# Kernel optimization log

Hardware: AMD Instinct MI355X
Metric: run time of the kernel (lower is better)

Reference implementation:

```python
import jax, jax.numpy as jnp
import numpy as np

MUL = 32
HEAD_DIM = 16
CLIP = 5.0
EPS = 1e-6
INV_SQRTD = 1.0 / np.sqrt(HEAD_DIM)
ENV_BLOCKS = (1, 3)          # 0e, 1o
TP_BLOCKS = (1, 1, 3, 3)     # 0e(0x0), 0e(1x1), 1o(0x1), 1o(1x0)


def so3_layernorm(x, g, block_dims):
    """x: [..., MUL, D]; per-irrep-block RMS norm over (mul, components), affine scale g [MUL, n_blocks]."""
    out, i = [], 0
    for b, d in enumerate(block_dims):
        blk = x[..., i:i + d]
        n = jnp.sqrt(jnp.mean(blk * blk, axis=(-2, -1), keepdims=True) + EPS)
        out.append(blk / n * g[:, b][:, None])
        i += d
    return jnp.concatenate(out, axis=-1)


def scatter_softmax(logits, seg, num_segments):
    """softmax over edges grouped by destination node. logits [E, M]."""
    m = jax.ops.segment_max(logits, seg, num_segments=num_segments)
    e = jnp.exp(logits - m[seg])
    d = jax.ops.segment_sum(e, seg, num_segments=num_segments)
    return e / d[seg]


def setup_inputs() -> dict:
    key = jax.random.key(0)
    ks = jax.random.split(key, 16)
    N, E, LAT, NODE_DIM, COND, HID = 16384, 262144, 64, 64, 32, 128
    sc = lambda f: f ** -0.5
    return {
        "node_attrs": jax.random.normal(ks[0], (N, NODE_DIM), jnp.float32),
        "scalar_state": jax.random.normal(ks[1], (E, LAT), jnp.float32),
        "equiv_state": jax.random.normal(ks[2], (E, MUL, 4), jnp.float32),
        "edge_conditioning": jax.random.normal(ks[3], (E, COND), jnp.float32),
        "residual_update_coeff": jax.random.uniform(ks[4], (1,), jnp.float32),
        "W_env1": jax.random.normal(ks[5], (LAT + COND, HID), jnp.float32) * sc(LAT + COND),
        "b_env1": jnp.zeros((HID,), jnp.float32),
        "W_env2": jax.random.normal(ks[6], (HID, MUL * 2), jnp.float32) * sc(HID),
        "Wq": jax.random.normal(ks[7], (NODE_DIM, MUL * HEAD_DIM), jnp.float32) * sc(NODE_DIM),
        "Wk": jax.random.normal(ks[8], (LAT, MUL * HEAD_DIM), jnp.float32) * sc(LAT),
        "g_env": jnp.ones((MUL, 2), jnp.float32),
        "g_tp": jnp.ones((MUL, 4), jnp.float32),
        "Wp1": jax.random.normal(ks[9], (MUL * 2 + COND, HID), jnp.float32) * sc(MUL * 2 + COND),
        "bp1": jnp.zeros((HID,), jnp.float32),
        "Wp2": jax.random.normal(ks[10], (HID, LAT + MUL * 4), jnp.float32) * sc(HID),
        "edge_src": jax.random.randint(ks[11], (E,), 0, N),
    }


def reference(node_attrs, scalar_state, equiv_state, edge_conditioning,
              residual_update_coeff, W_env1, b_env1, W_env2, Wq, Wk,
              g_env, g_tp, Wp1, bp1, Wp2, edge_src):
    N = node_attrs.shape[0]
    E = scalar_state.shape[0]
    LAT = scalar_state.shape[1]

    # --- env_embed_mlp: scalar MLP -> per-(mul, irrep-block) gates on equiv state ---
    x = jnp.concatenate([scalar_state, edge_conditioning], axis=-1)
    h = jax.nn.silu(x @ W_env1 + b_env1)
    w = (h @ W_env2).reshape(E, MUL, 2)                    # [E, mul, 2 blocks]
    w_exp = jnp.repeat(w, np.array(ENV_BLOCKS), axis=-1, total_repeat_length=4)
    env_edges = equiv_state * w_exp                        # [E, mul, 4]

    # --- attention: edge-gathered query, clipped logits, scatter softmax ---
    Q = (node_attrs[edge_src] @ Wq).reshape(E, MUL, HEAD_DIM)
    K = (scalar_state @ Wk).reshape(E, MUL, HEAD_DIM)
    logits = jnp.einsum('emd,emd->em', Q, K) * INV_SQRTD
    logits = jnp.clip(logits, -CLIP, CLIP)
    attn = scatter_softmax(logits, edge_src, N)            # [E, mul]
    env_edges = env_edges * attn[..., None]

    # --- scatter-sum to nodes, SO3 layernorm, gather back ---
    env_nodes = jax.ops.segment_sum(env_edges, edge_src, num_segments=N)  # [N, mul, 4]
    env_nodes = so3_layernorm(env_nodes, g_env, ENV_BLOCKS)
    edge_local_env = env_nodes[edge_src]                   # [E, mul, 4]

    # --- Contracter, uuu mode, instructions: 0x0->0, 1x1->0, 0x1->1, 1x0->1 ---
    s1, v1 = equiv_state[..., 0], equiv_state[..., 1:4]
    s2, v2 = edge_local_env[..., 0], edge_local_env[..., 1:4]
    o0a = s1 * s2                                          # 0e
    o0b = jnp.einsum('emi,emi->em', v1, v2) / np.sqrt(3.0) # 0e (CG of 1x1->0)
    o1a = s1[..., None] * v2                               # 1o
    o1b = v1 * s2[..., None]                               # 1o
    tp_out = jnp.concatenate([o0a[..., None], o0b[..., None], o1a, o1b], axis=-1)  # [E, mul, 8]
    tp_out = so3_layernorm(tp_out, g_tp, TP_BLOCKS)

    # --- projection: scalar MLP -> new scalar latent + per-path weights mixing equiv blocks ---
    scalars = tp_out[..., :2].reshape(E, MUL * 2)
    xp = jnp.concatenate([scalars, edge_conditioning], axis=-1)
    hp = jax.nn.silu(xp @ Wp1 + bp1)
    op = hp @ Wp2
    new_scalar = op[:, :LAT]
    pw = op[:, LAT:].reshape(E, MUL, 4)
    new_s = pw[..., 0] * tp_out[..., 0] + pw[..., 1] * tp_out[..., 1]
    new_v = pw[..., 2:3] * tp_out[..., 2:5] + pw[..., 3:4] * tp_out[..., 5:8]
    new_equiv = jnp.concatenate([new_s[..., None], new_v], axis=-1)  # [E, mul, 4]

    # --- residual streams ---
    c_old = jax.lax.rsqrt(residual_update_coeff ** 2 + 1.0)
    c_new = residual_update_coeff * c_old
    scalar_out = c_old * scalar_state + c_new * new_scalar
    equiv_out = c_old * equiv_state + c_new * new_equiv
    return scalar_out, equiv_out
```

## Files before the change

kernel.cpp:

```cpp
#include <hip/hip_runtime.h>
#include <math.h>

#define EPSF 1e-6f
#define STX 100
#define STH 132

__device__ __forceinline__ float silu_f(float x){ return x * (1.0f/(1.0f + __expf(-x))); }

__global__ __launch_bounds__(256) void k_qnode(
    const float* __restrict__ na, const float* __restrict__ Wq,
    float* __restrict__ qn)
{
  __shared__ float At[64*16];
  const int nb = blockIdx.x * 16;
  const int t = threadIdx.x;
  for (int f = t; f < 16*64; f += 256){ int n = f>>6, i = f&63; At[i*16+n] = na[(size_t)(nb+n)*64 + i]; }
  __syncthreads();
  float acc0[16], acc1[16];
#pragma unroll
  for (int n=0;n<16;n++){ acc0[n]=0.f; acc1[n]=0.f; }
  for (int i=0;i<64;i++){
    float w0 = Wq[(size_t)i*512 + t];
    float w1 = Wq[(size_t)i*512 + t + 256];
#pragma unroll
    for (int n=0;n<16;n++){ float a = At[i*16+n]; acc0[n] = fmaf(a,w0,acc0[n]); acc1[n] = fmaf(a,w1,acc1[n]); }
  }
#pragma unroll
  for (int n=0;n<16;n++){
    qn[(size_t)(nb+n)*512 + t]       = acc0[n];
    qn[(size_t)(nb+n)*512 + t + 256] = acc1[n];
  }
}

__global__ __launch_bounds__(256) void k_hist(
    const int* __restrict__ esrc, int E, int* __restrict__ cnt)
{
  int i = blockIdx.x*256 + threadIdx.x;
  if (i < E) atomicAdd(cnt + esrc[i], 1);
}

__global__ __launch_bounds__(1024) void k_scan(
    int* __restrict__ cnt_cur, int N, int* __restrict__ off)
{
  __shared__ int part[1024];
  const int t = threadIdx.x;
  const int ipt = (N + 1023) >> 10;
  int s = 0;
  for (int k=0;k<ipt;k++){ int i = t*ipt + k; if (i < N) s += cnt_cur[i]; }
  part[t] = s;
  __syncthreads();
  for (int d=1; d<1024; d<<=1){
    int v = (t >= d) ? part[t-d] : 0;
    __syncthreads();
    part[t] += v;
    __syncthreads();
  }
  int run = (t==0) ? 0 : part[t-1];
  for (int k=0;k<ipt;k++){
    int i = t*ipt + k;
    if (i < N){ int c = cnt_cur[i]; off[i] = run; cnt_cur[i] = run; run += c; }
  }
  if (t == 1023) off[N] = part[1023];
}

__global__ __launch_bounds__(256) void k_scatter(
    const int* __restrict__ esrc, int E, int* __restrict__ cur, int* __restrict__ perm)
{
  int i = blockIdx.x*256 + threadIdx.x;
  if (i < E){ int p = atomicAdd(cur + esrc[i], 1); perm[p] = i; }
}

__global__ __launch_bounds__(256,4) void k_edge1(
    const float* __restrict__ ssi, const float* __restrict__ cond,
    const int* __restrict__ esrc,
    const float* __restrict__ W1, const float* __restrict__ b1,
    const float* __restrict__ W2, const float* __restrict__ Wk,
    const float* __restrict__ qn,
    float* __restrict__ elw)
{
  __shared__ float Xs[32*STX];
  __shared__ float Hs[32*STH];
  __shared__ float lg[32*32];
  __shared__ int src_l[32];
  const int e0 = blockIdx.x * 32;
  const int t = threadIdx.x;
  const int r0 = (t>>5)*4;

  if (t < 32) src_l[t] = esrc[e0+t];
  for (int f=t; f<512; f+=256){ int r=f>>4, q=(f&15)*4;
    *(float4*)(Xs + r*STX + q) = *(const float4*)(ssi + (size_t)(e0+r)*64 + q); }
  { int f=t; int r=f>>3, q=(f&7)*4;
    *(float4*)(Xs + r*STX + 64 + q) = *(const float4*)(cond + (size_t)(e0+r)*32 + q); }
  __syncthreads();

  {
    const int c0 = (t&31)*4;
    float acc[4][4] = {};
    for (int i0=0;i0<96;i0+=4){
      float4 wv[4], xv[4];
#pragma unroll
      for (int k=0;k<4;k++) wv[k] = *(const float4*)(W1 + (size_t)(i0+k)*128 + c0);
#pragma unroll
      for (int rr=0;rr<4;rr++) xv[rr] = *(const float4*)(Xs + (r0+rr)*STX + i0);
#pragma unroll
      for (int rr=0;rr<4;rr++){
        const float xs[4] = {xv[rr].x,xv[rr].y,xv[rr].z,xv[rr].w};
#pragma unroll
        for (int k=0;k<4;k++){
          acc[rr][0] = fmaf(xs[k], wv[k].x, acc[rr][0]);
          acc[rr][1] = fmaf(xs[k], wv[k].y, acc[rr][1]);
          acc[rr][2] = fmaf(xs[k], wv[k].z, acc[rr][2]);
          acc[rr][3] = fmaf(xs[k], wv[k].w, acc[rr][3]);
        }
      }
    }
    const float4 bb = *(const float4*)(b1 + c0);
#pragma unroll
    for (int rr=0;rr<4;rr++){
      float4 h;
      h.x = silu_f(acc[rr][0]+bb.x); h.y = silu_f(acc[rr][1]+bb.y);
      h.z = silu_f(acc[rr][2]+bb.z); h.w = silu_f(acc[rr][3]+bb.w);
      *(float4*)(Hs + (r0+rr)*STH + c0) = h;
    }
  }
  __syncthreads();

  float wacc[4][2] = {};
  {
    const int c0 = (t&31)*2;
    for (int j0=0;j0<128;j0+=4){
      float2 w2[4]; float4 hv[4];
#pragma unroll
      for (int k=0;k<4;k++) w2[k] = *(const float2*)(W2 + (size_t)(j0+k)*64 + c0);
#pragma unroll
      for (int rr=0;rr<4;rr++) hv[rr] = *(const float4*)(Hs + (r0+rr)*STH + j0);
#pragma unroll
      for (int rr=0;rr<4;rr++){
        const float hs[4] = {hv[rr].x,hv[rr].y,hv[rr].z,hv[rr].w};
#pragma unroll
        for (int k=0;k<4;k++){
          wacc[rr][0] = fmaf(hs[k], w2[k].x, wacc[rr][0]);
          wacc[rr][1] = fmaf(hs[k], w2[k].y, wacc[rr][1]);
        }
      }
    }
  }
  __syncthreads();
  float* wl = Hs;
  {
    const int c0 = (t&31)*2;
#pragma unroll
    for (int rr=0;rr<4;rr++)
      *(float2*)(wl + (r0+rr)*66 + c0) = make_float2(wacc[rr][0], wacc[rr][1]);
  }

  for (int it=0; it<4; it++){
    const int c0k = (t&31)*4 + it*128;
    float acc[4][4] = {};
    for (int i0=0;i0<64;i0+=4){
      float4 wv[4], xv[4];
#pragma unroll
      for (int k=0;k<4;k++) wv[k] = *(const float4*)(Wk + (size_t)(i0+k)*512 + c0k);
#pragma unroll
      for (int rr=0;rr<4;rr++) xv[rr] = *(const float4*)(Xs + (r0+rr)*STX + i0);
#pragma unroll
      for (int rr=0;rr<4;rr++){
        const float xs[4] = {xv[rr].x,xv[rr].y,xv[rr].z,xv[rr].w};
#pragma unroll
        for (int k=0;k<4;k++){
          acc[rr][0] = fmaf(xs[k], wv[k].x, acc[rr][0]);
          acc[rr][1] = fmaf(xs[k], wv[k].y, acc[rr][1]);
          acc[rr][2] = fmaf(xs[k], wv[k].z, acc[rr][2]);
          acc[rr][3] = fmaf(xs[k], wv[k].w, acc[rr][3]);
        }
      }
    }
    const int m = ((t&31)>>2) + it*8;
#pragma unroll
    for (int rr=0;rr<4;rr++){
      const float4 q = *(const float4*)(qn + (size_t)src_l[r0+rr]*512 + c0k);
      float p = acc[rr][0]*q.x + acc[rr][1]*q.y + acc[rr][2]*q.z + acc[rr][3]*q.w;
      p += __shfl_xor(p, 1);
      p += __shfl_xor(p, 2);
      if ((t&3)==0) lg[(r0+rr)*32 + m] = p;
    }
  }
  __syncthreads();

  for (int f=t; f<1024; f+=256){
    int r=f>>5, m=f&31;
    float l = lg[f] * 0.25f;
    l = fminf(5.0f, fmaxf(-5.0f, l));
    const float el = __expf(l);
    const size_t b = (size_t)(e0+r)*96;
    elw[b + m]      = el;
    elw[b + 32 + m] = el * wl[r*66 + 2*m];
    elw[b + 64 + m] = el * wl[r*66 + 2*m+1];
  }
}

__global__ __launch_bounds__(128) void k_env(
    const float* __restrict__ elw, const float* __restrict__ equiv,
    const int* __restrict__ perm, const int* __restrict__ off,
    const float* __restrict__ g_env, float* __restrict__ envn)
{
  __shared__ float red[128];
  __shared__ float inv0s, inv1s;
  const int n = blockIdx.x, t = threadIdx.x;
  const int m = t>>2, c = t&3;
  const int j0 = off[n], j1 = off[n+1];
  float den = 0.f, acc = 0.f;
  for (int j=j0; j<j1; j++){
    const int pe = perm[j];
    const size_t b = (size_t)pe*96;
    const float el = elw[b + m];
    const float a  = elw[b + (c ? 64 : 32) + m];
    const float ev = equiv[((size_t)pe*32 + m)*4 + c];
    den += el;
    acc = fmaf(a, ev, acc);
  }
  const float x = (den > 0.f) ? acc/den : 0.f;
  red[t] = x*x;
  __syncthreads();
  if (t < 32){
    float p0 = red[4*t];
    float p1 = red[4*t+1]+red[4*t+2]+red[4*t+3];
#pragma unroll
    for (int k=1;k<32;k<<=1){ p0 += __shfl_xor(p0,k); p1 += __shfl_xor(p1,k); }
    if (t==0){ inv0s = 1.0f/sqrtf(p0*(1.0f/32.0f) + EPSF); inv1s = 1.0f/sqrtf(p1*(1.0f/96.0f) + EPSF); }
  }
  __syncthreads();
  const float g = g_env[m*2 + (c?1:0)];
  envn[(size_t)n*128 + t] = x * (c ? inv1s : inv0s) * g;
}

__global__ __launch_bounds__(256,4) void k_edge1_atm(
    const float* __restrict__ ssi, const float* __restrict__ cond,
    const float* __restrict__ equiv, const int* __restrict__ esrc,
    const float* __restrict__ W1, const float* __restrict__ b1,
    const float* __restrict__ W2, const float* __restrict__ Wk,
    const float* __restrict__ qn,
    float* __restrict__ denom, float* __restrict__ num)
{
  __shared__ float Xs[32*STX];
  __shared__ float Hs[32*STH];
  __shared__ float lg[32*32];
  __shared__ int src_l[32];
  const int e0 = blockIdx.x * 32;
  const int t = threadIdx.x;
  const int r0 = (t>>5)*4;

  if (t < 32) src_l[t] = esrc[e0+t];
  for (int f=t; f<512; f+=256){ int r=f>>4, q=(f&15)*4;
    *(float4*)(Xs + r*STX + q) = *(const float4*)(ssi + (size_t)(e0+r)*64 + q); }
  { int f=t; int r=f>>3, q=(f&7)*4;
    *(float4*)(Xs + r*STX + 64 + q) = *(const float4*)(cond + (size_t)(e0+r)*32 + q); }
  __syncthreads();

  {
    const int c0 = (t&31)*4;
    float acc[4][4] = {};
    for (int i0=0;i0<96;i0+=4){
      float4 wv[4], xv[4];
#pragma unroll
      for (int k=0;k<4;k++) wv[k] = *(const float4*)(W1 + (size_t)(i0+k)*128 + c0);
#pragma unroll
      for (int rr=0;rr<4;rr++) xv[rr] = *(const float4*)(Xs + (r0+rr)*STX + i0);
#pragma unroll
      for (int rr=0;rr<4;rr++){
        const float xs[4] = {xv[rr].x,xv[rr].y,xv[rr].z,xv[rr].w};
#pragma unroll
        for (int k=0;k<4;k++){
          acc[rr][0] = fmaf(xs[k], wv[k].x, acc[rr][0]);
          acc[rr][1] = fmaf(xs[k], wv[k].y, acc[rr][1]);
          acc[rr][2] = fmaf(xs[k], wv[k].z, acc[rr][2]);
          acc[rr][3] = fmaf(xs[k], wv[k].w, acc[rr][3]);
        }
      }
    }
    const float4 bb = *(const float4*)(b1 + c0);
#pragma unroll
    for (int rr=0;rr<4;rr++){
      float4 h;
      h.x = silu_f(acc[rr][0]+bb.x); h.y = silu_f(acc[rr][1]+bb.y);
      h.z = silu_f(acc[rr][2]+bb.z); h.w = silu_f(acc[rr][3]+bb.w);
      *(float4*)(Hs + (r0+rr)*STH + c0) = h;
    }
  }
  __syncthreads();

  float wacc[4][2] = {};
  {
    const int c0 = (t&31)*2;
    for (int j0=0;j0<128;j0+=4){
      float2 w2[4]; float4 hv[4];
#pragma unroll
      for (int k=0;k<4;k++) w2[k] = *(const float2*)(W2 + (size_t)(j0+k)*64 + c0);
#pragma unroll
      for (int rr=0;rr<4;rr++) hv[rr] = *(const float4*)(Hs + (r0+rr)*STH + j0);
#pragma unroll
      for (int rr=0;rr<4;rr++){
        const float hs[4] = {hv[rr].x,hv[rr].y,hv[rr].z,hv[rr].w};
#pragma unroll
        for (int k=0;k<4;k++){
          wacc[rr][0] = fmaf(hs[k], w2[k].x, wacc[rr][0]);
          wacc[rr][1] = fmaf(hs[k], w2[k].y, wacc[rr][1]);
        }
      }
    }
  }
  __syncthreads();
  float* wl = Hs;
  {
    const int c0 = (t&31)*2;
#pragma unroll
    for (int rr=0;rr<4;rr++)
      *(float2*)(wl + (r0+rr)*66 + c0) = make_float2(wacc[rr][0], wacc[rr][1]);
  }

  for (int it=0; it<4; it++){
    const int c0k = (t&31)*4 + it*128;
    float acc[4][4] = {};
    for (int i0=0;i0<64;i0+=4){
      float4 wv[4], xv[4];
#pragma unroll
      for (int k=0;k<4;k++) wv[k] = *(const float4*)(Wk + (size_t)(i0+k)*512 + c0k);
#pragma unroll
      for (int rr=0;rr<4;rr++) xv[rr] = *(const float4*)(Xs + (r0+rr)*STX + i0);
#pragma unroll
      for (int rr=0;rr<4;rr++){
        const float xs[4] = {xv[rr].x,xv[rr].y,xv[rr].z,xv[rr].w};
#pragma unroll
        for (int k=0;k<4;k++){
          acc[rr][0] = fmaf(xs[k], wv[k].x, acc[rr][0]);
          acc[rr][1] = fmaf(xs[k], wv[k].y, acc[rr][1]);
          acc[rr][2] = fmaf(xs[k], wv[k].z, acc[rr][2]);
          acc[rr][3] = fmaf(xs[k], wv[k].w, acc[rr][3]);
        }
      }
    }
    const int m = ((t&31)>>2) + it*8;
#pragma unroll
    for (int rr=0;rr<4;rr++){
      const float4 q = *(const float4*)(qn + (size_t)src_l[r0+rr]*512 + c0k);
      float p = acc[rr][0]*q.x + acc[rr][1]*q.y + acc[rr][2]*q.z + acc[rr][3]*q.w;
      p += __shfl_xor(p, 1);
      p += __shfl_xor(p, 2);
      if ((t&3)==0) lg[(r0+rr)*32 + m] = p;
    }
  }
  __syncthreads();

  for (int f=t; f<1024; f+=256){
    int r=f>>5, m=f&31;
    float l = lg[f] * 0.25f;
    l = fminf(5.0f, fmaxf(-5.0f, l));
    float el = __expf(l);
    lg[f] = el;
    atomicAdd(denom + (size_t)src_l[r]*32 + m, el);
  }
  __syncthreads();

  for (int f=t; f<1024; f+=256){
    int r=f>>5, m=f&31;
    const float el = lg[r*32+m];
    const float w0 = wl[r*66 + 2*m]   * el;
    const float w1 = wl[r*66 + 2*m+1] * el;
    const float4 ev = *(const float4*)(equiv + ((size_t)(e0+r)*32 + m)*4);
    float* np = num + (size_t)src_l[r]*128 + 4*m;
    atomicAdd(np+0, w0*ev.x);
    atomicAdd(np+1, w1*ev.y);
    atomicAdd(np+2, w1*ev.z);
    atomicAdd(np+3, w1*ev.w);
  }
}

__global__ __launch_bounds__(128) void k_dnorm(
    float* __restrict__ num, const float* __restrict__ denom,
    const float* __restrict__ g_env)
{
  __shared__ float red[128];
  __shared__ float inv0s, inv1s;
  const int n = blockIdx.x, t = threadIdx.x;
  const int m = t>>2, c = t&3;
  const float d = denom[(size_t)n*32+m];
  const float x = (d > 0.0f) ? num[(size_t)n*128+t]/d : 0.0f;
  red[t] = x*x;
  __syncthreads();
  if (t < 32){
    float p0 = red[4*t];
    float p1 = red[4*t+1]+red[4*t+2]+red[4*t+3];
#pragma unroll
    for (int k=1;k<32;k<<=1){ p0 += __shfl_xor(p0,k); p1 += __shfl_xor(p1,k); }
    if (t==0){ inv0s = 1.0f/sqrtf(p0*(1.0f/32.0f) + EPSF); inv1s = 1.0f/sqrtf(p1*(1.0f/96.0f) + EPSF); }
  }
  __syncthreads();
  const float g = g_env[m*2 + (c?1:0)];
  num[(size_t)n*128+t] = x * (c ? inv1s : inv0s) * g;
}

__global__ __launch_bounds__(256,3) void k_edge2(
    const float* __restrict__ ssi, const float* __restrict__ cond,
    const float* __restrict__ equiv, const int* __restrict__ esrc,
    const float* __restrict__ envn, const float* __restrict__ g_tp,
    const float* __restrict__ Wp1, const float* __restrict__ bp1,
    const float* __restrict__ Wp2, const float* __restrict__ ruc,
    float* __restrict__ outs, float* __restrict__ oute)
{
  __shared__ float envl[32*STH];
  __shared__ float Xp[32*STX];
  __shared__ float Hp[32*STH];
  __shared__ float inv_l[32*4];
  __shared__ int src_l[32];
  const int e0 = blockIdx.x * 32;
  const int t = threadIdx.x;
  const int r0 = (t>>5)*4;
  if (t < 32) src_l[t] = esrc[e0+t];
  __syncthreads();
  for (int f=t; f<1024; f+=256){ int r=f>>5, q=(f&31)*4;
    *(float4*)(envl + r*STH + q) = *(const float4*)(envn + (size_t)src_l[r]*128 + q); }
  { int f=t; int r=f>>3, q=(f&7)*4;
    *(float4*)(Xp + r*STX + 64 + q) = *(const float4*)(cond + (size_t)(e0+r)*32 + q); }
  __syncthreads();

  {
    const int r = t>>3, sub = t&7;
    float ss0=0,ss1=0,ss2=0,ss3=0;
#pragma unroll
    for (int mm=0;mm<4;mm++){
      const int m = sub*4+mm;
      const float4 e4 = *(const float4*)(equiv + ((size_t)(e0+r)*32 + m)*4);
      const float4 n4 = *(const float4*)(envl + r*STH + 4*m);
      const float tp0 = e4.x*n4.x;
      const float dv  = e4.y*n4.y + e4.z*n4.z + e4.w*n4.w;
      const float tp1 = dv*0.5773502691896258f;
      ss0 += tp0*tp0;
      ss1 += tp1*tp1;
      ss2 += e4.x*e4.x*(n4.y*n4.y + n4.z*n4.z + n4.w*n4.w);
      ss3 += n4.x*n4.x*(e4.y*e4.y + e4.z*e4.z + e4.w*e4.w);
    }
#pragma unroll
    for (int k=1;k<8;k<<=1){
      ss0 += __shfl_xor(ss0,k); ss1 += __shfl_xor(ss1,k);
      ss2 += __shfl_xor(ss2,k); ss3 += __shfl_xor(ss3,k);
    }
    if (sub == 0){
      inv_l[r*4+0] = 1.0f/sqrtf(ss0*(1.0f/32.0f) + EPSF);
      inv_l[r*4+1] = 1.0f/sqrtf(ss1*(1.0f/32.0f) + EPSF);
      inv_l[r*4+2] = 1.0f/sqrtf(ss2*(1.0f/96.0f) + EPSF);
      inv_l[r*4+3] = 1.0f/sqrtf(ss3*(1.0f/96.0f) + EPSF);
    }
  }
  __syncthreads();

  for (int f=t; f<2048; f+=256){
    const int r = f>>6, col = f&63, m = col>>1;
    const float4 e4 = *(const float4*)(equiv + ((size_t)(e0+r)*32 + m)*4);
    const float4 n4 = *(const float4*)(envl + r*STH + 4*m);
    float v;
    if (col & 1)
      v = (e4.y*n4.y + e4.z*n4.z + e4.w*n4.w)*0.5773502691896258f * inv_l[r*4+1] * g_tp[m*4+1];
    else
      v = e4.x*n4.x * inv_l[r*4+0] * g_tp[m*4+0];
    Xp[r*STX + col] = v;
  }
  __syncthreads();

  {
    const int c0 = (t&31)*4;
    float acc[4][4] = {};
    for (int i0=0;i0<96;i0+=4){
      float4 wv[4], xv[4];
#pragma unroll
      for (int k=0;k<4;k++) wv[k] = *(const float4*)(Wp1 + (size_t)(i0+k)*128 + c0);
#pragma unroll
      for (int rr=0;rr<4;rr++) xv[rr] = *(const float4*)(Xp + (r0+rr)*STX + i0);
#pragma unroll
      for (int rr=0;rr<4;rr++){
        const float xs[4] = {xv[rr].x,xv[rr].y,xv[rr].z,xv[rr].w};
#pragma unroll
        for (int k=0;k<4;k++){
          acc[rr][0] = fmaf(xs[k], wv[k].x, acc[rr][0]);
          acc[rr][1] = fmaf(xs[k], wv[k].y, acc[rr][1]);
          acc[rr][2] = fmaf(xs[k], wv[k].z, acc[rr][2]);
          acc[rr][3] = fmaf(xs[k], wv[k].w, acc[rr][3]);
        }
      }
    }
    const float4 bb = *(const float4*)(bp1 + c0);
#pragma unroll
    for (int rr=0;rr<4;rr++){
      float4 h;
      h.x = silu_f(acc[rr][0]+bb.x); h.y = silu_f(acc[rr][1]+bb.y);
      h.z = silu_f(acc[rr][2]+bb.z); h.w = silu_f(acc[rr][3]+bb.w);
      *(float4*)(Hp + (r0+rr)*STH + c0) = h;
    }
  }
  __syncthreads();

  const float rv = ruc[0];
  const float c_old = 1.0f/sqrtf(rv*rv + 1.0f);
  const float c_new = rv * c_old;

  {
    const int c0 = (t&31)*2;
    float acc[4][2] = {};
    for (int j0=0;j0<128;j0+=4){
      float2 w2[4]; float4 hv[4];
#pragma unroll
      for (int k=0;k<4;k++) w2[k] = *(const float2*)(Wp2 + (size_t)(j0+k)*192 + c0);
#pragma unroll
      for (int rr=0;rr<4;rr++) hv[rr] = *(const float4*)(Hp + (r0+rr)*STH + j0);
#pragma unroll
      for (int rr=0;rr<4;rr++){
        const float hs[4] = {hv[rr].x,hv[rr].y,hv[rr].z,hv[rr].w};
#pragma unroll
        for (int k=0;k<4;k++){
          acc[rr][0] = fmaf(hs[k], w2[k].x, acc[rr][0]);
          acc[rr][1] = fmaf(hs[k], w2[k].y, acc[rr][1]);
        }
      }
    }
#pragma unroll
    for (int rr=0;rr<4;rr++){
      const size_t e = (size_t)(e0+r0+rr);
      const float2 s2 = *(const float2*)(ssi + e*64 + c0);
      float2 o2; o2.x = c_old*s2.x + c_new*acc[rr][0]; o2.y = c_old*s2.y + c_new*acc[rr][1];
      *(float2*)(outs + e*64 + c0) = o2;
    }
  }

  {
    const int m = t&31;
    float acc[4][4] = {};
    for (int j0=0;j0<128;j0+=4){
      float4 w4[4]; float4 hv[4];
#pragma unroll
      for (int k=0;k<4;k++) w4[k] = *(const float4*)(Wp2 + (size_t)(j0+k)*192 + 64 + 4*m);
#pragma unroll
      for (int rr=0;rr<4;rr++) hv[rr] = *(const float4*)(Hp + (r0+rr)*STH + j0);
#pragma unroll
      for (int rr=0;rr<4;rr++){
        const float hs[4] = {hv[rr].x,hv[rr].y,hv[rr].z,hv[rr].w};
#pragma unroll
        for (int k=0;k<4;k++){
          acc[rr][0] = fmaf(hs[k], w4[k].x, acc[rr][0]);
          acc[rr][1] = fmaf(hs[k], w4[k].y, acc[rr][1]);
          acc[rr][2] = fmaf(hs[k], w4[k].z, acc[rr][2]);
          acc[rr][3] = fmaf(hs[k], w4[k].w, acc[rr][3]);
        }
      }
    }
    const float g2 = g_tp[m*4+2], g3 = g_tp[m*4+3];
#pragma unroll
    for (int rr=0;rr<4;rr++){
      const int r = r0+rr;
      const size_t e = (size_t)(e0+r);
      const float4 e4 = *(const float4*)(equiv + (e*32 + m)*4);
      const float4 n4 = *(const float4*)(envl + r*STH + 4*m);
      const float tpn0 = Xp[r*STX + 2*m];
      const float tpn1 = Xp[r*STX + 2*m+1];
      const float a2 = acc[rr][2]*inv_l[r*4+2]*g2;
      const float a3 = acc[rr][3]*inv_l[r*4+3]*g3;
      float4 o;
      o.x = c_old*e4.x + c_new*(acc[rr][0]*tpn0 + acc[rr][1]*tpn1);
      o.y = c_old*e4.y + c_new*(a2*(e4.x*n4.y) + a3*(e4.y*n4.x));
      o.z = c_old*e4.z + c_new*(a2*(e4.x*n4.z) + a3*(e4.z*n4.x));
      o.w = c_old*e4.w + c_new*(a2*(e4.x*n4.w) + a3*(e4.w*n4.x));
      *(float4*)(oute + e*128 + 4*m) = o;
    }
  }
}

extern "C" void kernel_launch(void* const* d_in, const int* in_sizes, int n_in,
                              void* d_out, int out_size, void* d_ws, size_t ws_size,
                              hipStream_t stream)
{
  const float* na   = (const float*)d_in[0];
  const float* ssi  = (const float*)d_in[1];
  const float* eqv  = (const float*)d_in[2];
  const float* cond = (const float*)d_in[3];
  const float* ruc  = (const float*)d_in[4];
  const float* W1   = (const float*)d_in[5];
  const float* b1   = (const float*)d_in[6];
  const float* W2   = (const float*)d_in[7];
  const float* Wq   = (const float*)d_in[8];
  const float* Wk   = (const float*)d_in[9];
  const float* ge   = (const float*)d_in[10];
  const float* gt   = (const float*)d_in[11];
  const float* Wp1  = (const float*)d_in[12];
  const float* bp1  = (const float*)d_in[13];
  const float* Wp2  = (const float*)d_in[14];
  const int*   esrc = (const int*)d_in[15];

  const int N = in_sizes[0] / 64;
  const int E = in_sizes[1] / 64;

  float* outs  = (float*)d_out;
  float* oute  = outs + (size_t)E*64;

  const size_t need = ((size_t)N*128 + (size_t)N*512 + (size_t)E*96) * sizeof(float)
                    + ((size_t)2*N + 1 + (size_t)E) * sizeof(int);

  if (ws_size >= need) {
    float* envn = (float*)d_ws;
    float* qn   = envn + (size_t)N*128;
    float* elw  = qn   + (size_t)N*512;
    int*   off  = (int*)(elw + (size_t)E*96);
    int*   cur  = off + (N + 1);
    int*   perm = cur + N;

    hipMemsetAsync(cur, 0, (size_t)N*sizeof(int), stream);
    k_qnode  <<<N/16, 256, 0, stream>>>(na, Wq, qn);
    k_hist   <<<(E+255)/256, 256, 0, stream>>>(esrc, E, cur);
    k_scan   <<<1, 1024, 0, stream>>>(cur, N, off);
    k_scatter<<<(E+255)/256, 256, 0, stream>>>(esrc, E, cur, perm);
    k_edge1  <<<E/32, 256, 0, stream>>>(ssi, cond, esrc, W1, b1, W2, Wk, qn, elw);
    k_env    <<<N, 128, 0, stream>>>(elw, eqv, perm, off, ge, envn);
    k_edge2  <<<E/32, 256, 0, stream>>>(ssi, cond, eqv, esrc, envn, gt, Wp1, bp1, Wp2, ruc, outs, oute);
  } else {
    float* denom = (float*)d_ws;
    float* num   = denom + (size_t)N*32;
    float* qn    = num   + (size_t)N*128;

    hipMemsetAsync(d_ws, 0, (size_t)N*160*sizeof(float), stream);
    k_qnode    <<<N/16, 256, 0, stream>>>(na, Wq, qn);
    k_edge1_atm<<<E/32, 256, 0, stream>>>(ssi, cond, eqv, esrc, W1, b1, W2, Wk, qn, denom, num);
    k_dnorm    <<<N, 128, 0, stream>>>(num, denom, ge);
    k_edge2    <<<E/32, 256, 0, stream>>>(ssi, cond, eqv, esrc, num, gt, Wp1, bp1, Wp2, ruc, outs, oute);
  }
}
```

Measured before the change: 1.372 ms.

## Process edges in source-sorted order so per-node gathers become contiguous

```diff
diff --git a/kernel.cpp b/kernel.cpp
--- a/kernel.cpp
+++ b/kernel.cpp
@@ -64,15 +64,16 @@
 }
 
 __global__ __launch_bounds__(256) void k_scatter(
-    const int* __restrict__ esrc, int E, int* __restrict__ cur, int* __restrict__ perm)
+    const int* __restrict__ esrc, int E, int* __restrict__ cur,
+    int* __restrict__ perm, int* __restrict__ ssrc)
 {
   int i = blockIdx.x*256 + threadIdx.x;
-  if (i < E){ int p = atomicAdd(cur + esrc[i], 1); perm[p] = i; }
+  if (i < E){ int s = esrc[i]; int p = atomicAdd(cur + s, 1); perm[p] = i; ssrc[p] = s; }
 }
 
 __global__ __launch_bounds__(256,4) void k_edge1(
     const float* __restrict__ ssi, const float* __restrict__ cond,
-    const int* __restrict__ esrc,
+    const int* __restrict__ perm, const int* __restrict__ ssrc,
     const float* __restrict__ W1, const float* __restrict__ b1,
     const float* __restrict__ W2, const float* __restrict__ Wk,
     const float* __restrict__ qn,
@@ -82,15 +83,17 @@
   __shared__ float Hs[32*STH];
   __shared__ float lg[32*32];
   __shared__ int src_l[32];
+  __shared__ int perm_l[32];
   const int e0 = blockIdx.x * 32;
   const int t = threadIdx.x;
   const int r0 = (t>>5)*4;
 
-  if (t < 32) src_l[t] = esrc[e0+t];
+  if (t < 32){ src_l[t] = ssrc[e0+t]; perm_l[t] = perm[e0+t]; }
+  __syncthreads();
   for (int f=t; f<512; f+=256){ int r=f>>4, q=(f&15)*4;
-    *(float4*)(Xs + r*STX + q) = *(const float4*)(ssi + (size_t)(e0+r)*64 + q); }
+    *(float4*)(Xs + r*STX + q) = *(const float4*)(ssi + (size_t)perm_l[r]*64 + q); }
   { int f=t; int r=f>>3, q=(f&7)*4;
-    *(float4*)(Xs + r*STX + 64 + q) = *(const float4*)(cond + (size_t)(e0+r)*32 + q); }
+    *(float4*)(Xs + r*STX + 64 + q) = *(const float4*)(cond + (size_t)perm_l[r]*32 + q); }
   __syncthreads();
 
   {
@@ -211,10 +214,10 @@
   const int j0 = off[n], j1 = off[n+1];
   float den = 0.f, acc = 0.f;
   for (int j=j0; j<j1; j++){
-    const int pe = perm[j];
-    const size_t b = (size_t)pe*96;
+    const size_t b = (size_t)j*96;
     const float el = elw[b + m];
     const float a  = elw[b + (c ? 64 : 32) + m];
+    const int pe = perm[j];
     const float ev = equiv[((size_t)pe*32 + m)*4 + c];
     den += el;
     acc = fmaf(a, ev, acc);
@@ -401,7 +404,8 @@
 
 __global__ __launch_bounds__(256,3) void k_edge2(
     const float* __restrict__ ssi, const float* __restrict__ cond,
-    const float* __restrict__ equiv, const int* __restrict__ esrc,
+    const float* __restrict__ equiv, const int* __restrict__ nsrc,
+    const int* __restrict__ eord,
     const float* __restrict__ envn, const float* __restrict__ g_tp,
     const float* __restrict__ Wp1, const float* __restrict__ bp1,
     const float* __restrict__ Wp2, const float* __restrict__ ruc,
@@ -412,24 +416,29 @@
   __shared__ float Hp[32*STH];
   __shared__ float inv_l[32*4];
   __shared__ int src_l[32];
+  __shared__ int perm_l[32];
   const int e0 = blockIdx.x * 32;
   const int t = threadIdx.x;
   const int r0 = (t>>5)*4;
-  if (t < 32) src_l[t] = esrc[e0+t];
+  if (t < 32){
+    src_l[t]  = nsrc[e0+t];
+    perm_l[t] = eord ? eord[e0+t] : (e0+t);
+  }
   __syncthreads();
   for (int f=t; f<1024; f+=256){ int r=f>>5, q=(f&31)*4;
     *(float4*)(envl + r*STH + q) = *(const float4*)(envn + (size_t)src_l[r]*128 + q); }
   { int f=t; int r=f>>3, q=(f&7)*4;
-    *(float4*)(Xp + r*STX + 64 + q) = *(const float4*)(cond + (size_t)(e0+r)*32 + q); }
+    *(float4*)(Xp + r*STX + 64 + q) = *(const float4*)(cond + (size_t)perm_l[r]*32 + q); }
   __syncthreads();
 
   {
     const int r = t>>3, sub = t&7;
+    const size_t pe = (size_t)perm_l[r];
     float ss0=0,ss1=0,ss2=0,ss3=0;
 #pragma unroll
     for (int mm=0;mm<4;mm++){
       const int m = sub*4+mm;
-      const float4 e4 = *(const float4*)(equiv + ((size_t)(e0+r)*32 + m)*4);
+      const float4 e4 = *(const float4*)(equiv + (pe*32 + m)*4);
       const float4 n4 = *(const float4*)(envl + r*STH + 4*m);
       const float tp0 = e4.x*n4.x;
       const float dv  = e4.y*n4.y + e4.z*n4.z + e4.w*n4.w;
@@ -455,7 +464,7 @@
 
   for (int f=t; f<2048; f+=256){
     const int r = f>>6, col = f&63, m = col>>1;
-    const float4 e4 = *(const float4*)(equiv + ((size_t)(e0+r)*32 + m)*4);
+    const float4 e4 = *(const float4*)(equiv + ((size_t)perm_l[r]*32 + m)*4);
     const float4 n4 = *(const float4*)(envl + r*STH + 4*m);
     float v;
     if (col & 1)
@@ -523,7 +532,7 @@
     }
 #pragma unroll
     for (int rr=0;rr<4;rr++){
-      const size_t e = (size_t)(e0+r0+rr);
+      const size_t e = (size_t)perm_l[r0+rr];
       const float2 s2 = *(const float2*)(ssi + e*64 + c0);
       float2 o2; o2.x = c_old*s2.x + c_new*acc[rr][0]; o2.y = c_old*s2.y + c_new*acc[rr][1];
       *(float2*)(outs + e*64 + c0) = o2;
@@ -555,7 +564,7 @@
 #pragma unroll
     for (int rr=0;rr<4;rr++){
       const int r = r0+rr;
-      const size_t e = (size_t)(e0+r);
+      const size_t e = (size_t)perm_l[r];
       const float4 e4 = *(const float4*)(equiv + (e*32 + m)*4);
       const float4 n4 = *(const float4*)(envl + r*STH + 4*m);
       const float tpn0 = Xp[r*STX + 2*m];
@@ -600,7 +609,7 @@
   float* oute  = outs + (size_t)E*64;
 
   const size_t need = ((size_t)N*128 + (size_t)N*512 + (size_t)E*96) * sizeof(float)
-                    + ((size_t)2*N + 1 + (size_t)E) * sizeof(int);
+                    + ((size_t)2*N + 1 + (size_t)2*E) * sizeof(int);
 
   if (ws_size >= need) {
     float* envn = (float*)d_ws;
@@ -609,15 +618,16 @@
     int*   off  = (int*)(elw + (size_t)E*96);
     int*   cur  = off + (N + 1);
     int*   perm = cur + N;
+    int*   ssrc = perm + E;
 
     hipMemsetAsync(cur, 0, (size_t)N*sizeof(int), stream);
     k_qnode  <<<N/16, 256, 0, stream>>>(na, Wq, qn);
     k_hist   <<<(E+255)/256, 256, 0, stream>>>(esrc, E, cur);
     k_scan   <<<1, 1024, 0, stream>>>(cur, N, off);
-    k_scatter<<<(E+255)/256, 256, 0, stream>>>(esrc, E, cur, perm);
-    k_edge1  <<<E/32, 256, 0, stream>>>(ssi, cond, esrc, W1, b1, W2, Wk, qn, elw);
+    k_scatter<<<(E+255)/256, 256, 0, stream>>>(esrc, E, cur, perm, ssrc);
+    k_edge1  <<<E/32, 256, 0, stream>>>(ssi, cond, perm, ssrc, W1, b1, W2, Wk, qn, elw);
     k_env    <<<N, 128, 0, stream>>>(elw, eqv, perm, off, ge, envn);
-    k_edge2  <<<E/32, 256, 0, stream>>>(ssi, cond, eqv, esrc, envn, gt, Wp1, bp1, Wp2, ruc, outs, oute);
+    k_edge2  <<<E/32, 256, 0, stream>>>(ssi, cond, eqv, ssrc, perm, envn, gt, Wp1, bp1, Wp2, ruc, outs, oute);
   } else {
     float* denom = (float*)d_ws;
     float* num   = denom + (size_t)N*32;
@@ -627,6 +637,6 @@
     k_qnode    <<<N/16, 256, 0, stream>>>(na, Wq, qn);
     k_edge1_atm<<<E/32, 256, 0, stream>>>(ssi, cond, eqv, esrc, W1, b1, W2, Wk, qn, denom, num);
     k_dnorm    <<<N, 128, 0, stream>>>(num, denom, ge);
-    k_edge2    <<<E/32, 256, 0, stream>>>(ssi, cond, eqv, esrc, num, gt, Wp1, bp1, Wp2, ruc, outs, oute);
-  }
-}
+    k_edge2    <<<E/32, 256, 0, stream>>>(ssi, cond, eqv, esrc, (const int*)nullptr, num, gt, Wp1, bp1, Wp2, ruc, outs, oute);
+  }
+}
```

Result: no change. 1.371 ms (-0.0%).
